# Kernel optimization log

Measured on AMD Instinct MI355X. Metric: run time of the kernel, lower is better.

Reference implementation:

```python
import jax, jax.numpy as jnp
import numpy as np


def setup_inputs() -> dict:
    key = jax.random.key(0)
    ks = jax.random.split(key, 5)
    B, T, D, H = 32, 2048, 512, 512
    return {
        "x": jax.random.normal(ks[0], (B, T, D), dtype=jnp.float32),
        "W_w": jax.random.normal(ks[1], (4 * H, D), dtype=jnp.float32) * 0.05,
        "W_b": jax.random.normal(ks[2], (4 * H,), dtype=jnp.float32) * 0.05,
        "U_w": jax.random.normal(ks[3], (4 * H, H), dtype=jnp.float32) * 0.05,
        "U_b": jax.random.normal(ks[4], (4 * H,), dtype=jnp.float32) * 0.05,
        "alpha": jnp.ones((H,), dtype=jnp.float32),
    }


def reference(x, W_w, W_b, U_w, U_b, alpha):
    B, T, D = x.shape
    H = alpha.shape[0]
    # Precompute input projection for all timesteps: [B, T, 4H]
    wx = jnp.einsum("btd,gd->btg", x, W_w) + W_b
    h0 = jnp.zeros((B, H), dtype=x.dtype)
    c0 = jnp.zeros((B, H), dtype=x.dtype)

    def step(carry, wx_t):
        h, c = carry
        gates = wx_t + h @ U_w.T + U_b  # [B, 4H]
        i, f, o, g = jnp.split(gates, 4, axis=-1)
        i = jax.nn.sigmoid(i)
        f = jax.nn.sigmoid(f)
        o = jax.nn.sigmoid(o)
        g = jnp.tanh(g)
        c = alpha * (f * c + i * g)
        h = o * jnp.tanh(c)
        return (h, c), h

    (h, c), outs = jax.lax.scan(step, (h0, c0), jnp.swapaxes(wx, 0, 1))
    outs = jnp.swapaxes(outs, 0, 1)  # [B, T, H]
    return outs, (h, c)
```

## Files before the change

### kernel.cpp

```cpp
#include <hip/hip_runtime.h>

#define TT 2048
#define BB 32
#define HH 512
#define NWG 32

typedef _Float16 half8 __attribute__((ext_vector_type(8)));
typedef float f32x4 __attribute__((ext_vector_type(4)));

__device__ __forceinline__ float fsig(float x) { return 1.f / (1.f + __expf(-x)); }
__device__ __forceinline__ float ftanh_(float x) {
  x = fminf(fmaxf(x, -15.f), 15.f);
  float e = __expf(2.f * x);
  return (e - 1.f) / (e + 1.f);
}

__global__ void cvt_f32_f16(const float* __restrict__ in, _Float16* __restrict__ out, int n4) {
  int i = blockIdx.x * 256 + threadIdx.x;
  if (i >= n4) return;
  float4 v = ((const float4*)in)[i];
  union { _Float16 h[4]; unsigned long long u; } r;
  r.h[0] = (_Float16)v.x; r.h[1] = (_Float16)v.y;
  r.h[2] = (_Float16)v.z; r.h[3] = (_Float16)v.w;
  ((unsigned long long*)out)[i] = r.u;
}

__global__ __launch_bounds__(256, 2) void gemm_wx(const _Float16* __restrict__ A,
                                                  const _Float16* __restrict__ Bw,
                                                  _Float16* __restrict__ C) {
  const int bn = blockIdx.x;
  const int bm = blockIdx.y;
  const int tid = threadIdx.x;
  const int lane = tid & 63;
  const int w = tid >> 6;
  __shared__ _Float16 As[128 * 40];
  __shared__ _Float16 Bs[128 * 40];
  const int moff = (w & 1) * 64;
  const int noff = (w >> 1) * 64;
  const int fm = lane & 15;
  const int kq = lane >> 4;
  f32x4 acc[4][4] = {};
  for (int kt = 0; kt < 16; ++kt) {
#pragma unroll
    for (int e = 0; e < 2; ++e) {
      int ci = tid * 2 + e;
      int r = ci >> 2, c16 = ci & 3;
      half8 av = *(const half8*)(A + (size_t)(bm * 128 + r) * 512 + kt * 32 + c16 * 8);
      half8 bv = *(const half8*)(Bw + (size_t)(bn * 128 + r) * 512 + kt * 32 + c16 * 8);
      *(half8*)(As + r * 40 + c16 * 8) = av;
      *(half8*)(Bs + r * 40 + c16 * 8) = bv;
    }
    __syncthreads();
    half8 af[4], bf[4];
#pragma unroll
    for (int i = 0; i < 4; ++i) {
      af[i] = *(const half8*)(As + (moff + i * 16 + fm) * 40 + kq * 8);
      bf[i] = *(const half8*)(Bs + (noff + i * 16 + fm) * 40 + kq * 8);
    }
#pragma unroll
    for (int i = 0; i < 4; ++i)
#pragma unroll
      for (int j = 0; j < 4; ++j)
        acc[i][j] = __builtin_amdgcn_mfma_f32_16x16x32_f16(af[i], bf[j], acc[i][j], 0, 0, 0);
    __syncthreads();
  }
#pragma unroll
  for (int i = 0; i < 4; ++i) {
    int row = bm * 128 + moff + i * 16 + (lane >> 4) * 4;
#pragma unroll
    for (int j = 0; j < 4; ++j) {
      int col = bn * 128 + noff + j * 16 + (lane & 15);
#pragma unroll
      for (int r = 0; r < 4; ++r)
        C[(size_t)(row + r) * 2048 + col] = (_Float16)acc[i][j][r];
    }
  }
}

__global__ __launch_bounds__(256, 1) void slstm_scan(
    const _Float16* __restrict__ wx,
    const _Float16* __restrict__ U16,
    const float* __restrict__ Wb, const float* __restrict__ Ub,
    const float* __restrict__ alpha,
    _Float16* __restrict__ hex,
    int* __restrict__ flags,
    float* __restrict__ out) {
  const int g = blockIdx.x;
  const int tid = threadIdx.x;
  const int lane = tid & 63;
  const int w = tid >> 6;
  const int mi = w & 1;
  const int qA = (w >> 1) * 2;
  const int ncol = lane & 15;
  const int kq = lane >> 4;
  const int am = mi * 16 + ncol;

  half8 Bf0[16], Bf1[16];
#pragma unroll
  for (int ks = 0; ks < 16; ++ks) {
    Bf0[ks] = *(const half8*)(U16 + (size_t)(qA * 512 + g * 16 + ncol) * 512 + ks * 32 + kq * 8);
    Bf1[ks] = *(const half8*)(U16 + (size_t)((qA + 1) * 512 + g * 16 + ncol) * 512 + ks * 32 + kq * 8);
  }

  const int eb = tid >> 3;
  const int jp = tid & 7;
  const int gj0 = g * 16 + jp * 2;
  float bias0[4], bias1[4];
#pragma unroll
  for (int q = 0; q < 4; ++q) {
    bias0[q] = Wb[q * 512 + gj0] + Ub[q * 512 + gj0];
    bias1[q] = Wb[q * 512 + gj0 + 1] + Ub[q * 512 + gj0 + 1];
  }
  const float al0 = alpha[gj0], al1 = alpha[gj0 + 1];
  float c0 = 0.f, c1 = 0.f;

  __shared__ float Sg[4 * 32 * 18];
  __shared__ _Float16 Swx[4 * 32 * 16];

  const int lq = tid >> 6;
  const int lb = (tid >> 1) & 31;
  const int lc = tid & 1;
  const _Float16* wxp = wx + (size_t)lb * TT * 2048 + lq * 512 + g * 16 + lc * 8;

  int spin_budget = 1 << 23;

  for (int t = 0; t < TT; ++t) {
    half8 wxv = *(const half8*)(wxp + (size_t)t * 2048);
    f32x4 acc0 = {0.f, 0.f, 0.f, 0.f}, acc1 = {0.f, 0.f, 0.f, 0.f};
    if (t > 0) {
      if (w == 0) {
        const int* fp = flags + (t - 1) * 16;
        while (__hip_atomic_load(fp, __ATOMIC_ACQUIRE, __HIP_MEMORY_SCOPE_AGENT) < NWG) {
          if (--spin_budget <= 0) break;
        }
      }
      __syncthreads();
      const _Float16* hb = hex + ((t & 1) ^ 1) * (BB * HH) + (size_t)am * HH + kq * 8;
#pragma unroll
      for (int ks = 0; ks < 16; ++ks) {
        half8 a = *(const half8*)(hb + ks * 32);
        acc0 = __builtin_amdgcn_mfma_f32_16x16x32_f16(a, Bf0[ks], acc0, 0, 0, 0);
        acc1 = __builtin_amdgcn_mfma_f32_16x16x32_f16(a, Bf1[ks], acc1, 0, 0, 0);
      }
    }
    *(half8*)(Swx + (lq * 32 + lb) * 16 + lc * 8) = wxv;
#pragma unroll
    for (int i = 0; i < 4; ++i) {
      int m = mi * 16 + kq * 4 + i;
      Sg[(qA * 32 + m) * 18 + ncol] = acc0[i];
      Sg[((qA + 1) * 32 + m) * 18 + ncol] = acc1[i];
    }
    __syncthreads();
    float p0[4], p1[4];
#pragma unroll
    for (int q = 0; q < 4; ++q) {
      const int so = (q * 32 + eb) * 18 + jp * 2;
      const int wo = (q * 32 + eb) * 16 + jp * 2;
      p0[q] = Sg[so] + (float)Swx[wo] + bias0[q];
      p1[q] = Sg[so + 1] + (float)Swx[wo + 1] + bias1[q];
    }
    float i0 = fsig(p0[0]), f0 = fsig(p0[1]), o0 = fsig(p0[2]), g0 = ftanh_(p0[3]);
    float i1 = fsig(p1[0]), f1 = fsig(p1[1]), o1 = fsig(p1[2]), g1 = ftanh_(p1[3]);
    c0 = al0 * (f0 * c0 + i0 * g0);
    c1 = al1 * (f1 * c1 + i1 * g1);
    float h0 = o0 * ftanh_(c0);
    float h1 = o1 * ftanh_(c1);
    union { _Float16 h[2]; unsigned int u; } pk;
    pk.h[0] = (_Float16)h0; pk.h[1] = (_Float16)h1;
    unsigned int* hx = (unsigned int*)hex + ((t & 1) * (BB * HH) + eb * HH + gj0) / 2;
    __hip_atomic_store(hx, pk.u, __ATOMIC_RELAXED, __HIP_MEMORY_SCOPE_AGENT);
    asm volatile("s_waitcnt vmcnt(0)" ::: "memory");
    __syncthreads();
    if (tid == 0)
      __hip_atomic_fetch_add(flags + t * 16, 1, __ATOMIC_RELEASE, __HIP_MEMORY_SCOPE_AGENT);
    size_t ob = ((size_t)eb * TT + t) * HH + gj0;
    __builtin_nontemporal_store(h0, out + ob);
    __builtin_nontemporal_store(h1, out + ob + 1);
    if (t == TT - 1) {
      const size_t HB = (size_t)BB * TT * HH;
      out[HB + eb * HH + gj0] = h0;
      out[HB + eb * HH + gj0 + 1] = h1;
      out[HB + BB * HH + eb * HH + gj0] = c0;
      out[HB + BB * HH + eb * HH + gj0 + 1] = c1;
    }
  }
}

extern "C" void kernel_launch(void* const* d_in, const int* in_sizes, int n_in,
                              void* d_out, int out_size, void* d_ws, size_t ws_size,
                              hipStream_t stream) {
  (void)in_sizes; (void)n_in; (void)out_size; (void)ws_size;
  const float* x  = (const float*)d_in[0];
  const float* Ww = (const float*)d_in[1];
  const float* Wb = (const float*)d_in[2];
  const float* Uw = (const float*)d_in[3];
  const float* Ub = (const float*)d_in[4];
  const float* al = (const float*)d_in[5];
  float* out = (float*)d_out;

  char* p = (char*)d_ws;
  _Float16* x16  = (_Float16*)p; p += (size_t)BB * TT * 512 * 2;
  _Float16* wx16 = (_Float16*)p; p += (size_t)BB * TT * 2048 * 2;
  _Float16* U16  = (_Float16*)p; p += (size_t)2048 * 512 * 2;
  _Float16* W16  = (_Float16*)p; p += (size_t)2048 * 512 * 2;
  _Float16* hexb = (_Float16*)p; p += (size_t)2 * BB * HH * 2;
  int* flags     = (int*)p;      p += (size_t)TT * 16 * 4;

  (void)hipMemsetAsync(flags, 0, (size_t)TT * 16 * 4, stream);
  cvt_f32_f16<<<32768, 256, 0, stream>>>(x, x16, BB * TT * 512 / 4);
  cvt_f32_f16<<<1024, 256, 0, stream>>>(Ww, W16, 2048 * 512 / 4);
  cvt_f32_f16<<<1024, 256, 0, stream>>>(Uw, U16, 2048 * 512 / 4);
  gemm_wx<<<dim3(16, 512), 256, 0, stream>>>(x16, W16, wx16);
  slstm_scan<<<NWG, 256, 0, stream>>>(wx16, U16, Wb, Ub, al, hexb, flags, out);
}
```

Before: 13.64 ms.

## Replace atomic-counter barrier with per-block flags polled by every wave

The grid-wide step barrier moves from one atomically incremented counter, polled by wave 0 and followed by __syncthreads, to one flag slot per workgroup. Every wave polls the 32 flags in parallel with a wave-wide vote and skips the block barrier. Hidden-state loads become relaxed atomic 64-bit loads so they bypass stale caches without acquire fences, and the two output stores are merged into one 8-byte nontemporal store. Dropping acquire/release ordering in favour of relaxed atomics plus an earlier vmcnt wait relies on hardware coherence behaviour, which is a memory-ordering risk.

```diff
diff --git a/kernel.cpp b/kernel.cpp
--- a/kernel.cpp
+++ b/kernel.cpp
@@ -123,24 +123,33 @@
   const _Float16* wxp = wx + (size_t)lb * TT * 2048 + lq * 512 + g * 16 + lc * 8;
 
   int spin_budget = 1 << 23;
+  const int fl = lane & 31;
 
   for (int t = 0; t < TT; ++t) {
     half8 wxv = *(const half8*)(wxp + (size_t)t * 2048);
     f32x4 acc0 = {0.f, 0.f, 0.f, 0.f}, acc1 = {0.f, 0.f, 0.f, 0.f};
     if (t > 0) {
-      if (w == 0) {
-        const int* fp = flags + (t - 1) * 16;
-        while (__hip_atomic_load(fp, __ATOMIC_ACQUIRE, __HIP_MEMORY_SCOPE_AGENT) < NWG) {
-          if (--spin_budget <= 0) break;
-        }
+      int* fp = flags + (size_t)(t - 1) * 32;
+      int v;
+      do {
+        v = __hip_atomic_load(fp + fl, __ATOMIC_RELAXED, __HIP_MEMORY_SCOPE_AGENT);
+        if (--spin_budget <= 0) break;
+      } while (!__all(v != 0));
+      asm volatile("" ::: "memory");
+      unsigned long long* hb64 =
+          (unsigned long long*)(hex + ((t & 1) ^ 1) * (BB * HH) + (size_t)am * HH);
+      union { unsigned long long u[2]; half8 h; } af[16];
+#pragma unroll
+      for (int ks = 0; ks < 16; ++ks) {
+        af[ks].u[0] = __hip_atomic_load(hb64 + ks * 8 + kq * 2,
+                                        __ATOMIC_RELAXED, __HIP_MEMORY_SCOPE_AGENT);
+        af[ks].u[1] = __hip_atomic_load(hb64 + ks * 8 + kq * 2 + 1,
+                                        __ATOMIC_RELAXED, __HIP_MEMORY_SCOPE_AGENT);
       }
-      __syncthreads();
-      const _Float16* hb = hex + ((t & 1) ^ 1) * (BB * HH) + (size_t)am * HH + kq * 8;
 #pragma unroll
       for (int ks = 0; ks < 16; ++ks) {
-        half8 a = *(const half8*)(hb + ks * 32);
-        acc0 = __builtin_amdgcn_mfma_f32_16x16x32_f16(a, Bf0[ks], acc0, 0, 0, 0);
-        acc1 = __builtin_amdgcn_mfma_f32_16x16x32_f16(a, Bf1[ks], acc1, 0, 0, 0);
+        acc0 = __builtin_amdgcn_mfma_f32_16x16x32_f16(af[ks].h, Bf0[ks], acc0, 0, 0, 0);
+        acc1 = __builtin_amdgcn_mfma_f32_16x16x32_f16(af[ks].h, Bf1[ks], acc1, 0, 0, 0);
       }
     }
     *(half8*)(Swx + (lq * 32 + lb) * 16 + lc * 8) = wxv;
@@ -172,10 +181,12 @@
     asm volatile("s_waitcnt vmcnt(0)" ::: "memory");
     __syncthreads();
     if (tid == 0)
-      __hip_atomic_fetch_add(flags + t * 16, 1, __ATOMIC_RELEASE, __HIP_MEMORY_SCOPE_AGENT);
+      __hip_atomic_store(flags + (size_t)t * 32 + g, 1,
+                         __ATOMIC_RELAXED, __HIP_MEMORY_SCOPE_AGENT);
     size_t ob = ((size_t)eb * TT + t) * HH + gj0;
-    __builtin_nontemporal_store(h0, out + ob);
-    __builtin_nontemporal_store(h1, out + ob + 1);
+    union { float f[2]; double d; } od;
+    od.f[0] = h0; od.f[1] = h1;
+    __builtin_nontemporal_store(od.d, (double*)(out + ob));
     if (t == TT - 1) {
       const size_t HB = (size_t)BB * TT * HH;
       out[HB + eb * HH + gj0] = h0;
@@ -204,9 +215,9 @@
   _Float16* U16  = (_Float16*)p; p += (size_t)2048 * 512 * 2;
   _Float16* W16  = (_Float16*)p; p += (size_t)2048 * 512 * 2;
   _Float16* hexb = (_Float16*)p; p += (size_t)2 * BB * HH * 2;
-  int* flags     = (int*)p;      p += (size_t)TT * 16 * 4;
-
-  (void)hipMemsetAsync(flags, 0, (size_t)TT * 16 * 4, stream);
+  int* flags     = (int*)p;      p += (size_t)TT * 32 * 4;
+
+  (void)hipMemsetAsync(flags, 0, (size_t)TT * 32 * 4, stream);
   cvt_f32_f16<<<32768, 256, 0, stream>>>(x, x16, BB * TT * 512 / 4);
   cvt_f32_f16<<<1024, 256, 0, stream>>>(Ww, W16, 2048 * 512 / 4);
   cvt_f32_f16<<<1024, 256, 0, stream>>>(Uw, U16, 2048 * 512 / 4);
```

New measurement: 12.21 ms. 1.12x faster.

## Replace flag barrier with tagged h-exchange words and per-lane gate compute

Applied to the files above, without the earlier changes.

The recurrent scan drops the global counter flag and block barriers. Each published h word now carries a timestep tag in its upper 32 bits, and consumers spin on the tagged loads directly, so arrival and data travel in a single agent-scope access. The workgroup shrinks to 128 threads, each computing all four gates for its own batch rows straight from MFMA accumulators, which removes the LDS staging and __syncthreads. The U weights are now reloaded from global memory every step instead of held in registers, trading memory traffic for lower register pressure and less synchronization.

```diff
diff --git a/kernel.cpp b/kernel.cpp
--- a/kernel.cpp
+++ b/kernel.cpp
@@ -77,111 +77,116 @@
   }
 }
 
-__global__ __launch_bounds__(256, 1) void slstm_scan(
+__global__ __launch_bounds__(128, 1) void slstm_scan(
     const _Float16* __restrict__ wx,
     const _Float16* __restrict__ U16,
     const float* __restrict__ Wb, const float* __restrict__ Ub,
     const float* __restrict__ alpha,
-    _Float16* __restrict__ hex,
-    int* __restrict__ flags,
+    unsigned long long* __restrict__ hexq,
     float* __restrict__ out) {
   const int g = blockIdx.x;
   const int tid = threadIdx.x;
   const int lane = tid & 63;
-  const int w = tid >> 6;
-  const int mi = w & 1;
-  const int qA = (w >> 1) * 2;
-  const int ncol = lane & 15;
+  const int mi = tid >> 6;
+  const int nc = lane & 15;
   const int kq = lane >> 4;
-  const int am = mi * 16 + ncol;
-
-  half8 Bf0[16], Bf1[16];
-#pragma unroll
-  for (int ks = 0; ks < 16; ++ks) {
-    Bf0[ks] = *(const half8*)(U16 + (size_t)(qA * 512 + g * 16 + ncol) * 512 + ks * 32 + kq * 8);
-    Bf1[ks] = *(const half8*)(U16 + (size_t)((qA + 1) * 512 + g * 16 + ncol) * 512 + ks * 32 + kq * 8);
-  }
-
-  const int eb = tid >> 3;
-  const int jp = tid & 7;
-  const int gj0 = g * 16 + jp * 2;
-  float bias0[4], bias1[4];
-#pragma unroll
-  for (int q = 0; q < 4; ++q) {
-    bias0[q] = Wb[q * 512 + gj0] + Ub[q * 512 + gj0];
-    bias1[q] = Wb[q * 512 + gj0 + 1] + Ub[q * 512 + gj0 + 1];
-  }
-  const float al0 = alpha[gj0], al1 = alpha[gj0 + 1];
-  float c0 = 0.f, c1 = 0.f;
-
-  __shared__ float Sg[4 * 32 * 18];
-  __shared__ _Float16 Swx[4 * 32 * 16];
-
-  const int lq = tid >> 6;
-  const int lb = (tid >> 1) & 31;
-  const int lc = tid & 1;
-  const _Float16* wxp = wx + (size_t)lb * TT * 2048 + lq * 512 + g * 16 + lc * 8;
-
-  int spin_budget = 1 << 23;
+  const int gcol = g * 16 + nc;
+  const int b0 = mi * 16 + kq * 4;
+  const int am = mi * 16 + nc;
+
+  float bias[4];
+#pragma unroll
+  for (int q = 0; q < 4; ++q) bias[q] = Wb[q * 512 + gcol] + Ub[q * 512 + gcol];
+  const float al = alpha[gcol];
+  float c[4] = {0.f, 0.f, 0.f, 0.f};
+
+  const _Float16* wxb[4];
+#pragma unroll
+  for (int i = 0; i < 4; ++i)
+    wxb[i] = wx + (size_t)(b0 + i) * TT * 2048 + gcol;
+
+  const _Float16* ub = U16 + (size_t)gcol * 512 + kq * 8;
+
+  int budget = 1 << 22;
 
   for (int t = 0; t < TT; ++t) {
-    half8 wxv = *(const half8*)(wxp + (size_t)t * 2048);
-    f32x4 acc0 = {0.f, 0.f, 0.f, 0.f}, acc1 = {0.f, 0.f, 0.f, 0.f};
+    _Float16 wxv[4][4];
+#pragma unroll
+    for (int i = 0; i < 4; ++i)
+#pragma unroll
+      for (int q = 0; q < 4; ++q)
+        wxv[i][q] = wxb[i][(size_t)t * 2048 + q * 512];
+
+    f32x4 acc[4] = {};
     if (t > 0) {
-      if (w == 0) {
-        const int* fp = flags + (t - 1) * 16;
-        while (__hip_atomic_load(fp, __ATOMIC_ACQUIRE, __HIP_MEMORY_SCOPE_AGENT) < NWG) {
-          if (--spin_budget <= 0) break;
+      const unsigned exp_tag = (unsigned)(t - 1);
+      const unsigned long long* hb =
+          hexq + (((t - 1) & 1) ? 8192 : 0) + (size_t)am * 256;
+      union { unsigned u[4]; half8 h; } af[16];
+      unsigned bad;
+      do {
+        bad = 0;
+#pragma unroll
+        for (int ks = 0; ks < 16; ++ks) {
+#pragma unroll
+          for (int p = 0; p < 4; ++p) {
+            unsigned long long wv = __hip_atomic_load(
+                hb + ks * 16 + kq * 4 + p, __ATOMIC_RELAXED, __HIP_MEMORY_SCOPE_AGENT);
+            bad |= ((unsigned)(wv >> 32)) ^ exp_tag;
+            af[ks].u[p] = (unsigned)wv;
+          }
+        }
+      } while (__any(bad != 0) && --budget > 0);
+#pragma unroll
+      for (int ks = 0; ks < 16; ++ks) {
+#pragma unroll
+        for (int q = 0; q < 4; ++q) {
+          half8 bf = *(const half8*)(ub + (size_t)q * 512 * 512 + ks * 32);
+          acc[q] = __builtin_amdgcn_mfma_f32_16x16x32_f16(af[ks].h, bf, acc[q], 0, 0, 0);
         }
       }
-      __syncthreads();
-      const _Float16* hb = hex + ((t & 1) ^ 1) * (BB * HH) + (size_t)am * HH + kq * 8;
-#pragma unroll
-      for (int ks = 0; ks < 16; ++ks) {
-        half8 a = *(const half8*)(hb + ks * 32);
-        acc0 = __builtin_amdgcn_mfma_f32_16x16x32_f16(a, Bf0[ks], acc0, 0, 0, 0);
-        acc1 = __builtin_amdgcn_mfma_f32_16x16x32_f16(a, Bf1[ks], acc1, 0, 0, 0);
-      }
-    }
-    *(half8*)(Swx + (lq * 32 + lb) * 16 + lc * 8) = wxv;
+    }
+    float h[4];
 #pragma unroll
     for (int i = 0; i < 4; ++i) {
-      int m = mi * 16 + kq * 4 + i;
-      Sg[(qA * 32 + m) * 18 + ncol] = acc0[i];
-      Sg[((qA + 1) * 32 + m) * 18 + ncol] = acc1[i];
-    }
-    __syncthreads();
-    float p0[4], p1[4];
-#pragma unroll
-    for (int q = 0; q < 4; ++q) {
-      const int so = (q * 32 + eb) * 18 + jp * 2;
-      const int wo = (q * 32 + eb) * 16 + jp * 2;
-      p0[q] = Sg[so] + (float)Swx[wo] + bias0[q];
-      p1[q] = Sg[so + 1] + (float)Swx[wo + 1] + bias1[q];
-    }
-    float i0 = fsig(p0[0]), f0 = fsig(p0[1]), o0 = fsig(p0[2]), g0 = ftanh_(p0[3]);
-    float i1 = fsig(p1[0]), f1 = fsig(p1[1]), o1 = fsig(p1[2]), g1 = ftanh_(p1[3]);
-    c0 = al0 * (f0 * c0 + i0 * g0);
-    c1 = al1 * (f1 * c1 + i1 * g1);
-    float h0 = o0 * ftanh_(c0);
-    float h1 = o1 * ftanh_(c1);
-    union { _Float16 h[2]; unsigned int u; } pk;
-    pk.h[0] = (_Float16)h0; pk.h[1] = (_Float16)h1;
-    unsigned int* hx = (unsigned int*)hex + ((t & 1) * (BB * HH) + eb * HH + gj0) / 2;
-    __hip_atomic_store(hx, pk.u, __ATOMIC_RELAXED, __HIP_MEMORY_SCOPE_AGENT);
-    asm volatile("s_waitcnt vmcnt(0)" ::: "memory");
-    __syncthreads();
-    if (tid == 0)
-      __hip_atomic_fetch_add(flags + t * 16, 1, __ATOMIC_RELEASE, __HIP_MEMORY_SCOPE_AGENT);
-    size_t ob = ((size_t)eb * TT + t) * HH + gj0;
-    __builtin_nontemporal_store(h0, out + ob);
-    __builtin_nontemporal_store(h1, out + ob + 1);
+      float pi = acc[0][i] + (float)wxv[i][0] + bias[0];
+      float pf = acc[1][i] + (float)wxv[i][1] + bias[1];
+      float po = acc[2][i] + (float)wxv[i][2] + bias[2];
+      float pg = acc[3][i] + (float)wxv[i][3] + bias[3];
+      float ig = fsig(pi), fg = fsig(pf), og = fsig(po), gg = ftanh_(pg);
+      c[i] = al * (fg * c[i] + ig * gg);
+      h[i] = og * ftanh_(c[i]);
+    }
+    union { _Float16 hh[2]; unsigned u; } pk01, pk23;
+    pk01.hh[0] = (_Float16)h[0]; pk01.hh[1] = (_Float16)h[1];
+    pk23.hh[0] = (_Float16)h[2]; pk23.hh[1] = (_Float16)h[3];
+    unsigned sw01 = (unsigned)__shfl_xor((int)pk01.u, 1);
+    unsigned sw23 = (unsigned)__shfl_xor((int)pk23.u, 1);
+    unsigned wA, wB; int bA, bB;
+    if ((lane & 1) == 0) {
+      wA = (pk01.u & 0xffffu) | ((sw01 & 0xffffu) << 16); bA = b0 + 0;
+      wB = (pk01.u >> 16)     | (sw01 & 0xffff0000u);     bB = b0 + 1;
+    } else {
+      wA = (sw23 & 0xffffu) | ((pk23.u & 0xffffu) << 16); bA = b0 + 2;
+      wB = (sw23 >> 16)     | (pk23.u & 0xffff0000u);     bB = b0 + 3;
+    }
+    const int cp = g * 8 + (nc >> 1);
+    unsigned long long* hw = hexq + ((t & 1) ? 8192 : 0);
+    const unsigned long long tagv = ((unsigned long long)(unsigned)t) << 32;
+    __hip_atomic_store(hw + (size_t)bA * 256 + cp, tagv | wA,
+                       __ATOMIC_RELAXED, __HIP_MEMORY_SCOPE_AGENT);
+    __hip_atomic_store(hw + (size_t)bB * 256 + cp, tagv | wB,
+                       __ATOMIC_RELAXED, __HIP_MEMORY_SCOPE_AGENT);
+#pragma unroll
+    for (int i = 0; i < 4; ++i)
+      __builtin_nontemporal_store(h[i], out + ((size_t)(b0 + i) * TT + t) * HH + gcol);
     if (t == TT - 1) {
       const size_t HB = (size_t)BB * TT * HH;
-      out[HB + eb * HH + gj0] = h0;
-      out[HB + eb * HH + gj0 + 1] = h1;
-      out[HB + BB * HH + eb * HH + gj0] = c0;
-      out[HB + BB * HH + eb * HH + gj0 + 1] = c1;
+#pragma unroll
+      for (int i = 0; i < 4; ++i) {
+        out[HB + (size_t)(b0 + i) * HH + gcol] = h[i];
+        out[HB + (size_t)BB * HH + (size_t)(b0 + i) * HH + gcol] = c[i];
+      }
     }
   }
 }
@@ -203,13 +208,13 @@
   _Float16* wx16 = (_Float16*)p; p += (size_t)BB * TT * 2048 * 2;
   _Float16* U16  = (_Float16*)p; p += (size_t)2048 * 512 * 2;
   _Float16* W16  = (_Float16*)p; p += (size_t)2048 * 512 * 2;
-  _Float16* hexb = (_Float16*)p; p += (size_t)2 * BB * HH * 2;
-  int* flags     = (int*)p;      p += (size_t)TT * 16 * 4;
-
-  (void)hipMemsetAsync(flags, 0, (size_t)TT * 16 * 4, stream);
+  unsigned long long* hexq = (unsigned long long*)p;
+  p += (size_t)2 * 32 * 256 * 8;
+
   cvt_f32_f16<<<32768, 256, 0, stream>>>(x, x16, BB * TT * 512 / 4);
   cvt_f32_f16<<<1024, 256, 0, stream>>>(Ww, W16, 2048 * 512 / 4);
   cvt_f32_f16<<<1024, 256, 0, stream>>>(Uw, U16, 2048 * 512 / 4);
   gemm_wx<<<dim3(16, 512), 256, 0, stream>>>(x16, W16, wx16);
-  slstm_scan<<<NWG, 256, 0, stream>>>(wx16, U16, Wb, Ub, al, hexb, flags, out);
-}
+  (void)hipMemsetAsync(hexq, 0xFF, (size_t)2 * 32 * 256 * 8, stream);
+  slstm_scan<<<NWG, 128, 0, stream>>>(wx16, U16, Wb, Ub, al, hexq, out);
+}
```

Measured after the change: 22.33 ms. 1.64x slower.
